# Optimization experiments

Measured on AMD Instinct MI355X. Metric: run time of the kernel, lower is better.

The kernel has to match this reference:

```python
import jax, jax.numpy as jnp
import numpy as np

IOU_THR = 0.5
SCORE_THR = 0.5
MAX_DET = 100
B, N, C = 16, 25200, 80


def setup_inputs() -> dict:
    key = jax.random.key(0)
    k1, k2, k3 = jax.random.split(key, 3)
    return {
        "boxes_xywh": jax.random.uniform(k1, (B, N, 4), dtype=jnp.float32),
        "objectness": jax.random.uniform(k2, (B, N, 1), dtype=jnp.float32),
        "class_prob": jax.random.uniform(k3, (B, N, C), dtype=jnp.float32),
    }


def _xywh_to_corners(b):
    x, y, w, h = jnp.split(b, 4, axis=-1)
    return jnp.concatenate([x - w / 2, y - h / 2, x + w / 2, y + h / 2], axis=-1)


def _broadcast_iou(box, boxes):
    # box [4], boxes [N,4] in x1,y1,x2,y2
    lt = jnp.maximum(box[:2], boxes[:, :2])
    rb = jnp.minimum(box[2:], boxes[:, 2:])
    wh = jnp.clip(rb - lt, 0.0)
    inter = wh[:, 0] * wh[:, 1]
    a1 = (box[2] - box[0]) * (box[3] - box[1])
    a2 = (boxes[:, 2] - boxes[:, 0]) * (boxes[:, 3] - boxes[:, 1])
    return inter / (a1 + a2 - inter + 1e-9)


def _nms_single(cand):
    # cand: [N, 4+1+C] rows = (x1,y1,x2,y2, score, class_probs...)
    n, d = cand.shape
    scores = cand[:, 4]
    active0 = scores >= SCORE_THR

    def body(i, state):
        active, out, count = state
        masked = jnp.where(active, scores, -jnp.inf)
        best = jnp.argmax(masked)
        valid = jnp.any(active)
        best_box = cand[best]
        out = out.at[i].set(jnp.where(valid, best_box, out[i]))
        count = count + valid.astype(jnp.int32)
        iou = _broadcast_iou(best_box[:4], cand[:, :4])
        keep = active & (iou <= IOU_THR)
        keep = keep.at[best].set(False)
        active = jnp.where(valid, keep, active)
        return active, out, count

    out0 = jnp.zeros((MAX_DET, d), cand.dtype)
    _, out, count = jax.lax.fori_loop(0, MAX_DET, body, (active0, out0, jnp.int32(0)))
    return out, count


def reference(boxes_xywh, objectness, class_prob):
    corners = _xywh_to_corners(boxes_xywh)  # [B,N,4]
    combined = jnp.concatenate([corners, objectness, class_prob], axis=-1)  # [B,N,5+C]
    final_result, count = jax.vmap(_nms_single)(combined)  # [B,MAX_DET,5+C], [B]
    nms_boxes = final_result[..., 0:4]
    nms_scores = final_result[..., 4:5]
    nms_classes = final_result[..., 5:]
    valid_count = count.astype(jnp.int32)[:, None]  # [B,1]
    return nms_boxes, nms_scores, nms_classes, valid_count
```

## Files before the change

kernel.cpp:

```cpp
#include <hip/hip_runtime.h>

#define NBOX    25200
#define NQ4     6300
#define NBATCH  16
#define NCLS    80
#define MAXDET  100
#define NBUCKET 1024
#define CAP     13824
#define SCORE_THR 0.5f
#define IOU_THR   0.5f
#define NGROUP  16

__device__ __forceinline__ void mk_corners(float x, float y, float w, float h,
                                           float& x1, float& y1, float& x2, float& y2) {
#pragma clang fp contract(off)
    float hw = w * 0.5f;
    float hh = h * 0.5f;
    x1 = x - hw; y1 = y - hh; x2 = x + hw; y2 = y + hh;
}

__device__ __forceinline__ float areaf(float x1, float y1, float x2, float y2) {
#pragma clang fp contract(off)
    return (x2 - x1) * (y2 - y1);
}

__device__ __forceinline__ bool iou_gt(float kx1, float ky1, float kx2, float ky2, float ka,
                                       float cx1, float cy1, float cx2, float cy2, float ca) {
#pragma clang fp contract(off)
    float lx = fmaxf(kx1, cx1);
    float ly = fmaxf(ky1, cy1);
    float rx = fminf(kx2, cx2);
    float ry = fminf(ky2, cy2);
    float w  = fmaxf(rx - lx, 0.0f);
    float h  = fmaxf(ry - ly, 0.0f);
    float inter = w * h;
    float denom = ka + ca - inter + 1e-9f;
    return (inter / denom) > IOU_THR;
}

__device__ __forceinline__ float readlane_f(float v, int j) {
    return __uint_as_float((unsigned)__builtin_amdgcn_readlane((int)__float_as_uint(v), j));
}

__global__ __launch_bounds__(1024)
void nms_kernel(const float* __restrict__ boxes_xywh,
                const float* __restrict__ objectness,
                const float* __restrict__ class_prob,
                float* __restrict__ out) {
    __shared__ unsigned s_hist[NBUCKET];
    __shared__ unsigned s_start[NBUCKET];
    __shared__ unsigned s_a[CAP];
    __shared__ unsigned s_b[CAP];
    __shared__ float4   s_kbox[MAXDET];
    __shared__ unsigned s_kept_idx[MAXDET];
    __shared__ unsigned s_wsum[16];
    __shared__ unsigned s_woff[16];
    __shared__ int      s_count;

    const int b = blockIdx.x;
    const int t = threadIdx.x;
    const int w = t >> 6;
    const int l = t & 63;
    const float* obj = objectness + (size_t)b * NBOX;
    const float* bx  = boxes_xywh + (size_t)b * NBOX * 4;

    float4 r[7];
#pragma unroll
    for (int i = 0; i < 7; ++i) {
        int n4 = t + (i << 10);
        if (n4 < NQ4) r[i] = *(const float4*)(obj + n4 * 4);
    }

    s_hist[t] = 0u;
    __syncthreads();
#pragma unroll
    for (int i = 0; i < 7; ++i) {
        int n4 = t + (i << 10);
        if (n4 < NQ4) {
            float sv[4] = {r[i].x, r[i].y, r[i].z, r[i].w};
#pragma unroll
            for (int u = 0; u < 4; ++u) {
                if (sv[u] >= SCORE_THR) {
                    unsigned ekey = __float_as_uint(sv[u]) - 0x3F000000u;
                    unsigned bkt  = ekey >> 13;
                    if (bkt > 1023u) bkt = 1023u;
                    atomicAdd(&s_hist[bkt], 1u);
                }
            }
        }
    }
    __syncthreads();

    {
        unsigned f = s_hist[1023 - t];
        unsigned v = f;
#pragma unroll
        for (int off = 1; off < 64; off <<= 1) {
            unsigned u = (unsigned)__shfl_up((int)v, off);
            if (l >= off) v += u;
        }
        if (l == 63) s_wsum[w] = v;
        __syncthreads();
        if (t < 64) {
            unsigned x = (t < 16) ? s_wsum[t] : 0u;
            unsigned y = x;
#pragma unroll
            for (int off = 1; off < 16; off <<= 1) {
                unsigned u = (unsigned)__shfl_up((int)y, off);
                if (t >= off) y += u;
            }
            if (t < 16) s_woff[t] = y - x;
        }
        __syncthreads();
        s_start[1023 - t] = v - f + s_woff[w];
    }
    if (t == 0) s_count = 0;
    __syncthreads();

#pragma unroll
    for (int i = 0; i < 7; ++i) {
        int n4 = t + (i << 10);
        if (n4 < NQ4) {
            float sv[4] = {r[i].x, r[i].y, r[i].z, r[i].w};
#pragma unroll
            for (int u = 0; u < 4; ++u) {
                if (sv[u] >= SCORE_THR) {
                    int n = n4 * 4 + u;
                    unsigned ekey = __float_as_uint(sv[u]) - 0x3F000000u;
                    unsigned bkt  = ekey >> 13;
                    if (bkt > 1023u) bkt = 1023u;
                    unsigned el = ekey - (bkt << 13);
                    if (el > 0x1FFFu) el = 0x1FFFu;
                    unsigned pos = atomicAdd(&s_start[bkt], 1u);
                    if (pos < CAP)
                        s_a[pos] = (el << 18) | (0x3FFFFu - (unsigned)n);
                }
            }
        }
    }
    __syncthreads();

    {
        float* oc = out + NBATCH * MAXDET * 5 + (size_t)b * MAXDET * NCLS;
        for (int e = t; e < MAXDET * NCLS; e += 1024) oc[e] = 0.0f;
    }

    auto sort_bucket = [&](int bkt) {
        unsigned h = s_hist[bkt];
        if (h == 0u) return;
        unsigned end = s_start[bkt];
        unsigned hi  = (end > CAP) ? CAP : end;
        unsigned lo  = (end >= h) ? end - h : 0u;
        if (lo > hi) lo = hi;
        unsigned sz = hi - lo;
        if (sz == 0u) return;
        if (sz <= 64u) {
            unsigned v = (l < (int)sz) ? s_a[lo + (unsigned)l] : 0u;
            int rank = 0;
            for (unsigned j = 0; j < sz; ++j)
                rank += ((unsigned)__shfl((int)v, (int)j) > v) ? 1 : 0;
            if (l < (int)sz) s_b[lo + (unsigned)rank] = v;
        } else {
            for (unsigned bb = 0; bb < sz; bb += 64u) {
                bool valid = bb + (unsigned)l < sz;
                unsigned v = valid ? s_a[lo + bb + (unsigned)l] : 0u;
                int rank = 0;
                for (unsigned j = 0; j < sz; ++j)
                    rank += (s_a[lo + j] > v) ? 1 : 0;
                if (valid) s_b[lo + (unsigned)rank] = v;
            }
        }
    };

    for (int bkt = (1023 - 63) + w; bkt <= 1023; bkt += 16) sort_bucket(bkt);
    __syncthreads();

    int count = 0;
    for (int g = 0; g < NGROUP; ++g) {
        const int BH = 1023 - (g << 6);
        const int BL = BH - 63;
        if (w == 0) {
            unsigned glo = (g == 0) ? 0u : s_start[BH + 1];
            unsigned ghi = s_start[BL];
            if (glo > CAP) glo = CAP;
            if (ghi > CAP) ghi = CAP;

            if (glo < ghi && count < MAXDET) {
                unsigned nidx = 0u; float4 nq = make_float4(0.f,0.f,0.f,0.f); float nsc = 0.f;
                {
                    int m0 = (int)(ghi - glo); if (m0 > 64) m0 = 64;
                    if (l < m0) {
                        unsigned p = s_b[glo + (unsigned)l];
                        nidx = 0x3FFFFu - (p & 0x3FFFFu);
                        nq = *(const float4*)(bx + (size_t)nidx * 4);
                        nsc = obj[nidx];
                    }
                }
                for (unsigned base = glo; base < ghi && count < MAXDET; base += 64u) {
                    int m = (int)(ghi - base); if (m > 64) m = 64;
                    unsigned cidx = nidx; float4 cq = nq; float csc = nsc;

                    unsigned nb = base + 64u;
                    if (nb < ghi) {
                        int nm = (int)(ghi - nb); if (nm > 64) nm = 64;
                        if (l < nm) {
                            unsigned p = s_b[nb + (unsigned)l];
                            nidx = 0x3FFFFu - (p & 0x3FFFFu);
                            nq = *(const float4*)(bx + (size_t)nidx * 4);
                            nsc = obj[nidx];
                        }
                    }

                    float cx1, cy1, cx2, cy2;
                    mk_corners(cq.x, cq.y, cq.z, cq.w, cx1, cy1, cx2, cy2);
                    float ca = areaf(cx1, cy1, cx2, cy2);

                    bool sup = (l >= m);
                    int k = 0;
                    for (; k + 8 <= count; k += 8) {
                        float4 kb[8];
#pragma unroll
                        for (int u = 0; u < 8; ++u) kb[u] = s_kbox[k + u];
#pragma unroll
                        for (int u = 0; u < 8; ++u) {
                            float kar = areaf(kb[u].x, kb[u].y, kb[u].z, kb[u].w);
                            sup = sup | iou_gt(kb[u].x, kb[u].y, kb[u].z, kb[u].w, kar,
                                               cx1, cy1, cx2, cy2, ca);
                        }
                    }
                    for (; k < count; ++k) {
                        float4 kb = s_kbox[k];
                        float kar = areaf(kb.x, kb.y, kb.z, kb.w);
                        sup = sup | iou_gt(kb.x, kb.y, kb.z, kb.w, kar, cx1, cy1, cx2, cy2, ca);
                    }
                    unsigned long long act = __ballot(!sup);

                    unsigned long long accmask = 0ull;
                    const int cbase = count;
                    while (act != 0ull && count < MAXDET) {
                        int j = (int)__builtin_ctzll(act);
                        accmask |= 1ull << j;
                        float bx1 = readlane_f(cx1, j), by1 = readlane_f(cy1, j);
                        float bx2 = readlane_f(cx2, j), by2 = readlane_f(cy2, j);
                        float bar = readlane_f(ca, j);
                        bool su = iou_gt(bx1, by1, bx2, by2, bar, cx1, cy1, cx2, cy2, ca);
                        ++count;
                        act &= ~(1ull << j);
                        act &= ~__ballot(su);
                    }

                    if (accmask & (1ull << l)) {
                        int slot = cbase + (int)__popcll(accmask & ((1ull << l) - 1ull));
                        s_kbox[slot] = make_float4(cx1, cy1, cx2, cy2);
                        s_kept_idx[slot] = cidx;
                        float* ob = out + ((size_t)b * MAXDET + slot) * 4;
                        ob[0] = cx1; ob[1] = cy1; ob[2] = cx2; ob[3] = cy2;
                        out[NBATCH * MAXDET * 4 + b * MAXDET + slot] = csc;
                    }
                    __asm__ volatile("s_waitcnt lgkmcnt(0)" ::: "memory");
                }
            }
            if (l == 0) s_count = count;
        } else if (g + 1 < NGROUP) {
            const int BH2 = BH - 64, BL2 = BH2 - 63;
            for (int bkt = BL2 + (w - 1); bkt <= BH2; bkt += 15) sort_bucket(bkt);
        }
        __syncthreads();
        if (s_count >= MAXDET) break;
    }

    const int count_f = s_count;
    for (int e = t; e < MAXDET * 4; e += 1024) {
        if ((e >> 2) >= count_f) out[(size_t)b * MAXDET * 4 + e] = 0.0f;
    }
    for (int i = t; i < MAXDET; i += 1024) {
        if (i >= count_f) out[NBATCH * MAXDET * 4 + b * MAXDET + i] = 0.0f;
    }
    const float* cp = class_prob + (size_t)b * NBOX * NCLS;
    float* oc = out + NBATCH * MAXDET * 5 + (size_t)b * MAXDET * NCLS;
    for (int e = t; e < count_f * NCLS; e += 1024) {
        int i = e / NCLS;
        int c = e - i * NCLS;
        oc[e] = cp[(size_t)s_kept_idx[i] * NCLS + c];
    }
    if (t == 0)
        out[NBATCH * MAXDET * 5 + NBATCH * MAXDET * NCLS + b] = (float)count_f;
}

extern "C" void kernel_launch(void* const* d_in, const int* in_sizes, int n_in,
                              void* d_out, int out_size, void* d_ws, size_t ws_size,
                              hipStream_t stream) {
    const float* boxes = (const float*)d_in[0];
    const float* objn  = (const float*)d_in[1];
    const float* clsp  = (const float*)d_in[2];
    float* out = (float*)d_out;
    nms_kernel<<<dim3(NBATCH), dim3(1024), 0, stream>>>(boxes, objn, clsp, out);
}
```

Measured before the change: 212.3 us.

## Scatter only top buckets eagerly, defer low-score scatter, deepen candidate prefetch

Only candidates in the top score buckets (>= LAZY_BKT) are scattered into the shared array up front. The remaining buckets are scattered on demand, by re-reading objectness, once the greedy loop reaches group nscat. This cuts atomic traffic in the common case where 100 detections are found early. The candidate prefetch becomes two batches deep, the keep-box inner loop is unrolled by 4 instead of 8, and zeroing of the class output moves to the end so it only covers unused rows. The deferred path adds a full re-read and extra barriers when it is needed.

```diff
diff --git a/kernel.cpp b/kernel.cpp
--- a/kernel.cpp
+++ b/kernel.cpp
@@ -10,6 +10,7 @@
 #define SCORE_THR 0.5f
 #define IOU_THR   0.5f
 #define NGROUP  16
+#define LAZY_BKT 896
 
 __device__ __forceinline__ void mk_corners(float x, float y, float w, float h,
                                            float& x1, float& y1, float& x2, float& y2) {
@@ -40,6 +41,10 @@
 
 __device__ __forceinline__ float readlane_f(float v, int j) {
     return __uint_as_float((unsigned)__builtin_amdgcn_readlane((int)__float_as_uint(v), j));
+}
+
+__device__ __forceinline__ unsigned score_key(float s) {
+    return __float_as_uint(s) - 0x3F000000u;
 }
 
 __global__ __launch_bounds__(1024)
@@ -81,8 +86,7 @@
 #pragma unroll
             for (int u = 0; u < 4; ++u) {
                 if (sv[u] >= SCORE_THR) {
-                    unsigned ekey = __float_as_uint(sv[u]) - 0x3F000000u;
-                    unsigned bkt  = ekey >> 13;
+                    unsigned bkt = score_key(sv[u]) >> 13;
                     if (bkt > 1023u) bkt = 1023u;
                     atomicAdd(&s_hist[bkt], 1u);
                 }
@@ -125,25 +129,21 @@
 #pragma unroll
             for (int u = 0; u < 4; ++u) {
                 if (sv[u] >= SCORE_THR) {
-                    int n = n4 * 4 + u;
-                    unsigned ekey = __float_as_uint(sv[u]) - 0x3F000000u;
+                    unsigned ekey = score_key(sv[u]);
                     unsigned bkt  = ekey >> 13;
                     if (bkt > 1023u) bkt = 1023u;
-                    unsigned el = ekey - (bkt << 13);
-                    if (el > 0x1FFFu) el = 0x1FFFu;
-                    unsigned pos = atomicAdd(&s_start[bkt], 1u);
-                    if (pos < CAP)
-                        s_a[pos] = (el << 18) | (0x3FFFFu - (unsigned)n);
+                    if (bkt >= LAZY_BKT) {
+                        int n = n4 * 4 + u;
+                        unsigned el = ekey & 0x1FFFu;
+                        unsigned pos = atomicAdd(&s_start[bkt], 1u);
+                        if (pos < CAP)
+                            s_a[pos] = (el << 18) | (0x3FFFFu - (unsigned)n);
+                    }
                 }
             }
         }
     }
     __syncthreads();
-
-    {
-        float* oc = out + NBATCH * MAXDET * 5 + (size_t)b * MAXDET * NCLS;
-        for (int e = t; e < MAXDET * NCLS; e += 1024) oc[e] = 0.0f;
-    }
 
     auto sort_bucket = [&](int bkt) {
         unsigned h = s_hist[bkt];
@@ -176,9 +176,37 @@
     __syncthreads();
 
     int count = 0;
+    int nscat = 2;
     for (int g = 0; g < NGROUP; ++g) {
         const int BH = 1023 - (g << 6);
         const int BL = BH - 63;
+
+        if (g >= nscat) {
+            for (int n4 = t; n4 < NQ4; n4 += 1024) {
+                float4 s4 = *(const float4*)(obj + n4 * 4);
+                float sv[4] = {s4.x, s4.y, s4.z, s4.w};
+#pragma unroll
+                for (int u = 0; u < 4; ++u) {
+                    if (sv[u] >= SCORE_THR) {
+                        unsigned ekey = score_key(sv[u]);
+                        unsigned bkt  = ekey >> 13;
+                        if (bkt > 1023u) bkt = 1023u;
+                        if (bkt < LAZY_BKT) {
+                            int n = n4 * 4 + u;
+                            unsigned el = ekey & 0x1FFFu;
+                            unsigned pos = atomicAdd(&s_start[bkt], 1u);
+                            if (pos < CAP)
+                                s_a[pos] = (el << 18) | (0x3FFFFu - (unsigned)n);
+                        }
+                    }
+                }
+            }
+            __syncthreads();
+            nscat = NGROUP;
+            for (int bkt = BL + w; bkt <= BH; bkt += 16) sort_bucket(bkt);
+            __syncthreads();
+        }
+
         if (w == 0) {
             unsigned glo = (g == 0) ? 0u : s_start[BH + 1];
             unsigned ghi = s_start[BL];
@@ -186,52 +214,48 @@
             if (ghi > CAP) ghi = CAP;
 
             if (glo < ghi && count < MAXDET) {
-                unsigned nidx = 0u; float4 nq = make_float4(0.f,0.f,0.f,0.f); float nsc = 0.f;
-                {
-                    int m0 = (int)(ghi - glo); if (m0 > 64) m0 = 64;
-                    if (l < m0) {
-                        unsigned p = s_b[glo + (unsigned)l];
-                        nidx = 0x3FFFFu - (p & 0x3FFFFu);
-                        nq = *(const float4*)(bx + (size_t)nidx * 4);
-                        nsc = obj[nidx];
-                    }
-                }
+                unsigned aidx, bidx; float4 aq, bq; float asc, bsc;
+                auto loadc = [&](unsigned cb, unsigned& ix, float4& q, float& sc) {
+                    ix = 0u; q = make_float4(0.f, 0.f, 0.f, 0.f); sc = 0.f;
+                    unsigned p0 = cb + (unsigned)l;
+                    if (p0 < ghi) {
+                        unsigned p = s_b[p0];
+                        ix = 0x3FFFFu - (p & 0x3FFFFu);
+                        q = *(const float4*)(bx + (size_t)ix * 4);
+                        sc = obj[ix];
+                    }
+                };
+                loadc(glo, aidx, aq, asc);
+                loadc(glo + 64u, bidx, bq, bsc);
+
                 for (unsigned base = glo; base < ghi && count < MAXDET; base += 64u) {
+                    unsigned cidx = aidx; float4 cq = aq; float csc = asc;
+                    aidx = bidx; aq = bq; asc = bsc;
+                    loadc(base + 128u, bidx, bq, bsc);
+
                     int m = (int)(ghi - base); if (m > 64) m = 64;
-                    unsigned cidx = nidx; float4 cq = nq; float csc = nsc;
-
-                    unsigned nb = base + 64u;
-                    if (nb < ghi) {
-                        int nm = (int)(ghi - nb); if (nm > 64) nm = 64;
-                        if (l < nm) {
-                            unsigned p = s_b[nb + (unsigned)l];
-                            nidx = 0x3FFFFu - (p & 0x3FFFFu);
-                            nq = *(const float4*)(bx + (size_t)nidx * 4);
-                            nsc = obj[nidx];
-                        }
-                    }
-
                     float cx1, cy1, cx2, cy2;
                     mk_corners(cq.x, cq.y, cq.z, cq.w, cx1, cy1, cx2, cy2);
                     float ca = areaf(cx1, cy1, cx2, cy2);
 
                     bool sup = (l >= m);
                     int k = 0;
-                    for (; k + 8 <= count; k += 8) {
-                        float4 kb[8];
-#pragma unroll
-                        for (int u = 0; u < 8; ++u) kb[u] = s_kbox[k + u];
-#pragma unroll
-                        for (int u = 0; u < 8; ++u) {
-                            float kar = areaf(kb[u].x, kb[u].y, kb[u].z, kb[u].w);
-                            sup = sup | iou_gt(kb[u].x, kb[u].y, kb[u].z, kb[u].w, kar,
-                                               cx1, cy1, cx2, cy2, ca);
-                        }
+                    for (; k + 4 <= count; k += 4) {
+                        float4 kb0 = s_kbox[k],     kb1 = s_kbox[k + 1];
+                        float4 kb2 = s_kbox[k + 2], kb3 = s_kbox[k + 3];
+                        sup = sup | iou_gt(kb0.x, kb0.y, kb0.z, kb0.w,
+                                           areaf(kb0.x, kb0.y, kb0.z, kb0.w), cx1, cy1, cx2, cy2, ca);
+                        sup = sup | iou_gt(kb1.x, kb1.y, kb1.z, kb1.w,
+                                           areaf(kb1.x, kb1.y, kb1.z, kb1.w), cx1, cy1, cx2, cy2, ca);
+                        sup = sup | iou_gt(kb2.x, kb2.y, kb2.z, kb2.w,
+                                           areaf(kb2.x, kb2.y, kb2.z, kb2.w), cx1, cy1, cx2, cy2, ca);
+                        sup = sup | iou_gt(kb3.x, kb3.y, kb3.z, kb3.w,
+                                           areaf(kb3.x, kb3.y, kb3.z, kb3.w), cx1, cy1, cx2, cy2, ca);
                     }
                     for (; k < count; ++k) {
                         float4 kb = s_kbox[k];
-                        float kar = areaf(kb.x, kb.y, kb.z, kb.w);
-                        sup = sup | iou_gt(kb.x, kb.y, kb.z, kb.w, kar, cx1, cy1, cx2, cy2, ca);
+                        sup = sup | iou_gt(kb.x, kb.y, kb.z, kb.w,
+                                           areaf(kb.x, kb.y, kb.z, kb.w), cx1, cy1, cx2, cy2, ca);
                     }
                     unsigned long long act = __ballot(!sup);
 
@@ -261,7 +285,7 @@
                 }
             }
             if (l == 0) s_count = count;
-        } else if (g + 1 < NGROUP) {
+        } else if (g + 1 < NGROUP && g + 1 < nscat) {
             const int BH2 = BH - 64, BL2 = BH2 - 63;
             for (int bkt = BL2 + (w - 1); bkt <= BH2; bkt += 15) sort_bucket(bkt);
         }
@@ -269,22 +293,23 @@
         if (s_count >= MAXDET) break;
     }
 
-    const int count_f = s_count;
+    const int cf = s_count;
     for (int e = t; e < MAXDET * 4; e += 1024) {
-        if ((e >> 2) >= count_f) out[(size_t)b * MAXDET * 4 + e] = 0.0f;
+        if ((e >> 2) >= cf) out[(size_t)b * MAXDET * 4 + e] = 0.0f;
     }
     for (int i = t; i < MAXDET; i += 1024) {
-        if (i >= count_f) out[NBATCH * MAXDET * 4 + b * MAXDET + i] = 0.0f;
+        if (i >= cf) out[NBATCH * MAXDET * 4 + b * MAXDET + i] = 0.0f;
     }
     const float* cp = class_prob + (size_t)b * NBOX * NCLS;
     float* oc = out + NBATCH * MAXDET * 5 + (size_t)b * MAXDET * NCLS;
-    for (int e = t; e < count_f * NCLS; e += 1024) {
+    for (int e = t; e < cf * NCLS; e += 1024) {
         int i = e / NCLS;
         int c = e - i * NCLS;
         oc[e] = cp[(size_t)s_kept_idx[i] * NCLS + c];
     }
+    for (int e = t + cf * NCLS; e < MAXDET * NCLS; e += 1024) oc[e] = 0.0f;
     if (t == 0)
-        out[NBATCH * MAXDET * 5 + NBATCH * MAXDET * NCLS + b] = (float)count_f;
+        out[NBATCH * MAXDET * 5 + NBATCH * MAXDET * NCLS + b] = (float)cf;
 }
 
 extern "C" void kernel_launch(void* const* d_in, const int* in_sizes, int n_in,
```

Result: faster. 198.3 us (-6.6%).
